# Kernel optimization log

Measured on AMD Instinct MI355X. Metric: run time of the kernel, lower is better.

## Reference

```python
import jax, jax.numpy as jnp
import numpy as np

L, B, T, C, H, V = 6, 8, 1024, 1024, 16, 4096
HS = C // H  # head size = 64


def _ln(x, g, b):
    mu = x.mean(-1, keepdims=True)
    var = ((x - mu) ** 2).mean(-1, keepdims=True)
    return (x - mu) * jax.lax.rsqrt(var + 1e-5) * g + b


def setup_inputs() -> dict:
    key = jax.random.key(0)
    ks = jax.random.split(key, 12)
    s = 0.02
    return {
        "idx": jax.random.randint(ks[0], (B, T), 0, V),
        "tok_emb": jax.random.normal(ks[1], (V, C), jnp.float32) * s,
        "pos_emb": jax.random.normal(ks[2], (T, C), jnp.float32) * s,
        "Wq": jax.random.normal(ks[3], (L, C, C), jnp.float32) * s,
        "Wk": jax.random.normal(ks[4], (L, C, C), jnp.float32) * s,
        "Wv": jax.random.normal(ks[5], (L, C, C), jnp.float32) * s,
        "Wo": jax.random.normal(ks[6], (L, C, C), jnp.float32) * s,
        "bo": jnp.zeros((L, C), jnp.float32),
        "ln1_g": jnp.ones((L, C), jnp.float32),
        "ln1_b": jnp.zeros((L, C), jnp.float32),
        "ln2_g": jnp.ones((L, C), jnp.float32),
        "ln2_b": jnp.zeros((L, C), jnp.float32),
        "W1": jax.random.normal(ks[7], (L, C, 4 * C), jnp.float32) * s,
        "b1": jnp.zeros((L, 4 * C), jnp.float32),
        "W2": jax.random.normal(ks[8], (L, 4 * C, C), jnp.float32) * s,
        "b2": jnp.zeros((L, C), jnp.float32),
        "lnf_g": jnp.ones((C,), jnp.float32),
        "lnf_b": jnp.zeros((C,), jnp.float32),
        "lm_w": jax.random.normal(ks[9], (C, V), jnp.float32) * s,
        "lm_b": jnp.zeros((V,), jnp.float32),
    }


def _gpt(idx, tok_emb, pos_emb, Wq, Wk, Wv, Wo, bo, ln1_g, ln1_b, ln2_g, ln2_b,
         W1, b1, W2, b2, lnf_g, lnf_b, lm_w, lm_b):
    x = tok_emb[idx] + pos_emb[None, :idx.shape[1]]  # (B,T,C)
    mask = jnp.tril(jnp.ones((T, T), bool))
    neg_inf = jnp.float32(-jnp.inf)

    def block(x, p):
        wq, wk, wv, wo, bo_, g1, be1, g2, be2, w1, bb1, w2, bb2 = p
        h = _ln(x, g1, be1)
        # per-head projections (no bias), heads concatenated along feature dim
        q = (h @ wq).reshape(B, T, H, HS)
        k = (h @ wk).reshape(B, T, H, HS)
        v = (h @ wv).reshape(B, T, H, HS)
        # NOTE: faithful to source -- scores are MULTIPLIED by sqrt(head_size)
        att = jnp.einsum('bqhd,bkhd->bhqk', q, k) * (HS ** 0.5)
        att = jnp.where(mask, att, neg_inf)
        p_att = jax.nn.softmax(att, axis=-1)  # dropout is identity at eval
        o = jnp.einsum('bhqk,bkhd->bqhd', p_att, v).reshape(B, T, C)
        x = x + o @ wo + bo_
        h2 = _ln(x, g2, be2)
        x = x + jax.nn.relu(h2 @ w1 + bb1) @ w2 + bb2
        return x, None

    x, _ = jax.lax.scan(
        block, x,
        (Wq, Wk, Wv, Wo, bo, ln1_g, ln1_b, ln2_g, ln2_b, W1, b1, W2, b2))
    x = _ln(x, lnf_g, lnf_b)
    return x @ lm_w + lm_b  # logits (B,T,V)


def reference(idx, tok_emb, pos_emb, Wq, Wk, Wv, Wo, bo, ln1_g, ln1_b, ln2_g,
              ln2_b, W1, b1, W2, b2, lnf_g, lnf_b, lm_w, lm_b):
    return _gpt(idx, tok_emb, pos_emb, Wq, Wk, Wv, Wo, bo, ln1_g, ln1_b,
                ln2_g, ln2_b, W1, b1, W2, b2, lnf_g, lnf_b, lm_w, lm_b)
```

## Files before the change

### kernel.cpp

```cpp
#include <hip/hip_runtime.h>

#define LL 6
#define BB 8
#define TT 1024
#define CC 1024
#define HH 16
#define HS 64
#define VV 4096
#define BT (BB*TT)

typedef __attribute__((ext_vector_type(4))) float f32x4;
typedef __attribute__((ext_vector_type(8))) short bf16x8;

#define RAWBAR() do { \
  asm volatile("s_waitcnt lgkmcnt(0)" ::: "memory"); \
  __builtin_amdgcn_s_barrier(); \
  __builtin_amdgcn_sched_barrier(0); \
} while (0)

__device__ __forceinline__ float bf2f(unsigned short u) {
  union { unsigned int u; float f; } v; v.u = ((unsigned int)u) << 16; return v.f;
}
__device__ __forceinline__ unsigned short rne16(float f) {
  unsigned u = __float_as_uint(f);
  return (unsigned short)((u + 0x7fffu + ((u >> 16) & 1u)) >> 16);
}
__device__ __forceinline__ void gld16(const uint4* g, uint4* l) {
  __builtin_amdgcn_global_load_lds(
      (const __attribute__((address_space(1))) void*)g,
      (__attribute__((address_space(3))) void*)l, 16, 0, 0);
}

__global__ __launch_bounds__(256) void embed_kernel(
    const int* __restrict__ idx, const float* __restrict__ tok,
    const float* __restrict__ pos, float* __restrict__ x) {
  int bt = blockIdx.x;
  int t = bt & (TT - 1);
  int id = idx[bt];
  float4 te = reinterpret_cast<const float4*>(tok)[(size_t)id * (CC/4) + threadIdx.x];
  float4 pe = reinterpret_cast<const float4*>(pos)[(size_t)t * (CC/4) + threadIdx.x];
  float4 r; r.x = te.x+pe.x; r.y = te.y+pe.y; r.z = te.z+pe.z; r.w = te.w+pe.w;
  reinterpret_cast<float4*>(x)[(size_t)bt * (CC/4) + threadIdx.x] = r;
}

struct Oct2 { uint4 p0, p1; };
__device__ __forceinline__ Oct2 split8_rne2(const float* f) {
  unsigned h0[8], h1[8];
  #pragma unroll
  for (int e = 0; e < 8; ++e) {
    h0[e] = rne16(f[e]);
    float r = f[e] - bf2f((unsigned short)h0[e]);
    h1[e] = rne16(r);
  }
  Oct2 o;
  o.p0 = make_uint4(h0[0]|(h0[1]<<16), h0[2]|(h0[3]<<16), h0[4]|(h0[5]<<16), h0[6]|(h0[7]<<16));
  o.p1 = make_uint4(h1[0]|(h1[1]<<16), h1[2]|(h1[3]<<16), h1[4]|(h1[5]<<16), h1[6]|(h1[7]<<16));
  return o;
}
__device__ __forceinline__ uint4 pack8_rne(const float* f) {
  unsigned h[8];
  #pragma unroll
  for (int e = 0; e < 8; ++e) h[e] = rne16(f[e]);
  return make_uint4(h[0]|(h[1]<<16), h[2]|(h[3]<<16), h[4]|(h[5]<<16), h[6]|(h[7]<<16));
}

__global__ __launch_bounds__(256) void lnsplit_kernel(
    const float* __restrict__ x, const float* __restrict__ g,
    const float* __restrict__ b, uint4* __restrict__ outp) {
  __shared__ float red[8];
  __shared__ float rowbuf[1024];
  int row = blockIdx.x, tid = threadIdx.x;
  float4 v = reinterpret_cast<const float4*>(x)[(size_t)row * (CC/4) + tid];
  float s  = v.x+v.y+v.z+v.w;
  float ss = v.x*v.x+v.y*v.y+v.z*v.z+v.w*v.w;
  #pragma unroll
  for (int off = 32; off; off >>= 1) { s += __shfl_xor(s, off); ss += __shfl_xor(ss, off); }
  if ((tid & 63) == 0) { red[tid>>6] = s; red[4+(tid>>6)] = ss; }
  __syncthreads();
  s  = red[0]+red[1]+red[2]+red[3];
  ss = red[4]+red[5]+red[6]+red[7];
  float mu = s * (1.f/CC);
  float rs = rsqrtf(ss*(1.f/CC) - mu*mu + 1e-5f);
  float4 gg = reinterpret_cast<const float4*>(g)[tid];
  float4 bb = reinterpret_cast<const float4*>(b)[tid];
  float4 o;
  o.x = (v.x-mu)*rs*gg.x + bb.x;
  o.y = (v.y-mu)*rs*gg.y + bb.y;
  o.z = (v.z-mu)*rs*gg.z + bb.z;
  o.w = (v.w-mu)*rs*gg.w + bb.w;
  *reinterpret_cast<float4*>(&rowbuf[tid*4]) = o;
  __syncthreads();
  if (tid < 128) {
    const size_t aPS = (size_t)128 * 16 * 512;
    int kt = tid >> 3, sl = tid & 7;
    int r = row & 63, mt = row >> 6;
    float f[8];
    #pragma unroll
    for (int e = 0; e < 8; ++e) f[e] = rowbuf[tid*8 + e];
    size_t di = ((size_t)(mt*16 + kt))*512 + r*8 + (sl ^ (r & 7));
    Oct2 ot = split8_rne2(f);
    outp[di] = ot.p0; outp[aPS+di] = ot.p1;
  }
}

__global__ __launch_bounds__(256) void lnsplit1_kernel(
    const float* __restrict__ x, const float* __restrict__ g,
    const float* __restrict__ b, uint4* __restrict__ outp) {
  __shared__ float red[8];
  __shared__ float rowbuf[1024];
  int row = blockIdx.x, tid = threadIdx.x;
  float4 v = reinterpret_cast<const float4*>(x)[(size_t)row * (CC/4) + tid];
  float s  = v.x+v.y+v.z+v.w;
  float ss = v.x*v.x+v.y*v.y+v.z*v.z+v.w*v.w;
  #pragma unroll
  for (int off = 32; off; off >>= 1) { s += __shfl_xor(s, off); ss += __shfl_xor(ss, off); }
  if ((tid & 63) == 0) { red[tid>>6] = s; red[4+(tid>>6)] = ss; }
  __syncthreads();
  s  = red[0]+red[1]+red[2]+red[3];
  ss = red[4]+red[5]+red[6]+red[7];
  float mu = s * (1.f/CC);
  float rs = rsqrtf(ss*(1.f/CC) - mu*mu + 1e-5f);
  float4 gg = reinterpret_cast<const float4*>(g)[tid];
  float4 bb = reinterpret_cast<const float4*>(b)[tid];
  float4 o;
  o.x = (v.x-mu)*rs*gg.x + bb.x;
  o.y = (v.y-mu)*rs*gg.y + bb.y;
  o.z = (v.z-mu)*rs*gg.z + bb.z;
  o.w = (v.w-mu)*rs*gg.w + bb.w;
  *reinterpret_cast<float4*>(&rowbuf[tid*4]) = o;
  __syncthreads();
  if (tid < 128) {
    int kt = tid >> 3, sl = tid & 7;
    int r = row & 63, mt = row >> 6;
    float f[8];
    #pragma unroll
    for (int e = 0; e < 8; ++e) f[e] = rowbuf[tid*8 + e];
    size_t di = ((size_t)(mt*16 + kt))*512 + r*8 + (sl ^ (r & 7));
    outp[di] = pack8_rne(f);
  }
}

__global__ __launch_bounds__(256) void bsplit4_kernel(
    const float* __restrict__ Wq, const float* __restrict__ Wk,
    const float* __restrict__ Wv, const float* __restrict__ Wo,
    uint4* __restrict__ bsQK, uint4* __restrict__ bsV, uint4* __restrict__ bsO) {
  int z = blockIdx.z;
  const float* Bw = (z == 0) ? Wq : (z == 1) ? Wk : (z == 2) ? Wv : Wo;
  uint4* outp = (z <= 1) ? bsQK : (z == 2) ? bsV : bsO;
  int ntile0 = (z == 1) ? 8 : 0;
  int ntTotal = (z <= 1) ? 16 : 8;
  int ntile = ntile0 + blockIdx.x, kt = blockIdx.y;
  size_t planeStride = (size_t)ntTotal * 16 * 1024;
  int tid = threadIdx.x;
  int bcol = tid & 127, bkcg = tid >> 7;
  #pragma unroll
  for (int g = 0; g < 4; ++g) {
    int kc = bkcg*4 + g;
    float f[8];
    #pragma unroll
    for (int j = 0; j < 8; ++j)
      f[j] = Bw[(size_t)(kt*64 + kc*8 + j) * CC + blockIdx.x*128 + bcol];
    size_t di = (((size_t)ntile * 16 + kt) * 8 + kc) * 128 + bcol;
    Oct2 o = split8_rne2(f);
    outp[di] = o.p0; outp[planeStride+di] = o.p1;
  }
}

template<int NP>
__global__ __launch_bounds__(256) void bsplit_kernel(
    const float* __restrict__ Bw, uint4* __restrict__ outp, int ldb,
    int ntile0, int ntTotal) {
  int ntile = ntile0 + blockIdx.x, kt = blockIdx.y;
  size_t planeStride = (size_t)ntTotal * gridDim.y * 1024;
  int tid = threadIdx.x;
  int bcol = tid & 127, bkcg = tid >> 7;
  #pragma unroll
  for (int g = 0; g < 4; ++g) {
    int kc = bkcg*4 + g;
    float f[8];
    #pragma unroll
    for (int j = 0; j < 8; ++j)
      f[j] = Bw[(size_t)(kt*64 + kc*8 + j) * ldb + blockIdx.x*128 + bcol];
    size_t di = (((size_t)ntile * gridDim.y + kt) * 8 + kc) * 128 + bcol;
    if (NP == 2) {
      Oct2 o = split8_rne2(f);
      outp[di] = o.p0; outp[planeStride+di] = o.p1;
    } else {
      outp[di] = pack8_rne(f);
    }
  }
}

template<int NP, bool ASP, int NM>
__global__ __launch_bounds__(256) void gemm128_kernel(
    const float* __restrict__ A, int lda,
    const uint4* __restrict__ Asp, size_t aPS,
    const uint4* __restrict__ Bs,
    const float* __restrict__ bias, const float* __restrict__ res,
    float* __restrict__ outf, int K, int ldc, int relu,
    int ntile0, int ntTotal, int kt0, int ktTotal, int vtmode,
    uint4* __restrict__ kout) {
  __shared__ uint4 lds_all[NP*2048];
  uint4* lds_a = lds_all;
  uint4* lds_b = lds_all + NP*1024;
  int tid = threadIdx.x;
  int NYd8 = gridDim.y >> 3;
  int li = blockIdx.x + gridDim.x * blockIdx.y;
  int xcd = li & 7, j = li >> 3;
  int by = xcd + 8 * (j % NYd8);
  int bx = j / NYd8;
  int m0 = by * 128;
  int n0 = bx * 128;
  int ntg = ntile0 + bx;
  size_t bPS = (size_t)ntTotal * ktTotal * 1024;
  int lane = tid & 63, w = tid >> 6;
  int wm = w >> 1, wn = w & 1;
  int lr = lane & 15, lk = lane >> 4;
  int nkt = K >> 6;

  f32x4 acc[4][4];
  #pragma unroll
  for (int m = 0; m < 4; ++m)
    #pragma unroll
    for (int n = 0; n < 4; ++n)
      acc[m][n] = (f32x4){0.f, 0.f, 0.f, 0.f};

  for (int kt = 0; kt < nkt; ++kt) {
    if (ASP) {
      #pragma unroll
      for (int p = 0; p < NP; ++p) {
        const uint4* s0 = Asp + p*aPS + ((size_t)(2*by)   * nkt + kt)*512;
        const uint4* s1 = Asp + p*aPS + ((size_t)(2*by+1) * nkt + kt)*512;
        #pragma unroll
        for (int i = 0; i < 2; ++i) {
          int ch = w*2 + i;
          gld16(s0 + ch*64 + lane, &lds_a[p*1024 + ch*64]);
          gld16(s1 + ch*64 + lane, &lds_a[p*1024 + 512 + ch*64]);
        }
      }
    } else {
      #pragma unroll
      for (int i = 0; i < 4; ++i) {
        int c = tid + i * 256;
        int row = c >> 3, sl = c & 7;
        const float4* ap = reinterpret_cast<const float4*>(
            A + (size_t)(m0+row)*lda + kt*64 + sl*8);
        float4 x0 = ap[0], x1 = ap[1];
        float f[8] = {x0.x,x0.y,x0.z,x0.w,x1.x,x1.y,x1.z,x1.w};
        int di = (row>>6)*512 + (row&63)*8 + (sl ^ (row & 7));
        if (NP == 2) {
          Oct2 o = split8_rne2(f);
          lds_a[di] = o.p0; lds_a[1024 + di] = o.p1;
        } else {
          lds_a[di] = pack8_rne(f);
        }
      }
    }
    {
      int ktg = kt0 + kt;
      #pragma unroll
      for (int p = 0; p < NP; ++p) {
        const uint4* sb = Bs + p*bPS + ((size_t)ntg * ktTotal + ktg)*1024;
        #pragma unroll
        for (int i = 0; i < 4; ++i) {
          int ch = w*4 + i;
          gld16(sb + ch*64 + lane, &lds_b[p*1024 + ch*64]);
        }
      }
    }
    __syncthreads();
    #pragma unroll
    for (int ks = 0; ks < 2; ++ks) {
      int kc = ks*4 + lk;
      bf16x8 af[NP][4], bfr[NP][4];
      #pragma unroll
      for (int m = 0; m < 4; ++m) {
        int row = wm*64 + m*16 + lr;
        int si = (row>>6)*512 + (row&63)*8 + (kc ^ (row & 7));
        #pragma unroll
        for (int p = 0; p < NP; ++p)
          af[p][m] = reinterpret_cast<const bf16x8*>(lds_a + p*1024)[si];
      }
      #pragma unroll
      for (int n = 0; n < 4; ++n) {
        int si = kc*128 + wn*64 + n*16 + lr;
        #pragma unroll
        for (int p = 0; p < NP; ++p)
          bfr[p][n] = reinterpret_cast<const bf16x8*>(lds_b + p*1024)[si];
      }
      #pragma unroll
      for (int m = 0; m < 4; ++m)
        #pragma unroll
        for (int n = 0; n < 4; ++n) {
          acc[m][n] = __builtin_amdgcn_mfma_f32_16x16x32_bf16(af[0][m], bfr[0][n], acc[m][n], 0, 0, 0);
          if (NP == 2) {
            acc[m][n] = __builtin_amdgcn_mfma_f32_16x16x32_bf16(af[0][m], bfr[1][n], acc[m][n], 0, 0, 0);
            acc[m][n] = __builtin_amdgcn_mfma_f32_16x16x32_bf16(af[1][m], bfr[0][n], acc[m][n], 0, 0, 0);
            if (NM == 4)
              acc[m][n] = __builtin_amdgcn_mfma_f32_16x16x32_bf16(af[1][m], bfr[1][n], acc[m][n], 0, 0, 0);
          }
        }
    }
    __syncthreads();
  }

  if (vtmode == 1) {
    char* vb = (char*)outf;
    const size_t VPSb = (size_t)2048 * 512 * 16;
    #pragma unroll
    for (int m = 0; m < 4; ++m) {
      int row = m0 + wm*64 + m*16 + lk*4;
      int bq = row >> 10;
      int t  = row & (TT-1);
      int ktile = t >> 6, r = t & 63;
      int kc = r >> 3, toct0 = r & 7;
      #pragma unroll
      for (int n = 0; n < 4; ++n) {
        int col = n0 + wn*64 + n*16 + lr;
        int hh2 = col >> 6, d = col & 63;
        int tile = (bq*HH + hh2)*16 + ktile;
        int vi = kc*64 + ((d ^ (kc<<1)) & 63);
        unsigned p0[4], p1[4];
        #pragma unroll
        for (int j2 = 0; j2 < 4; ++j2) {
          float v = acc[m][n][j2];
          p0[j2] = rne16(v);
          p1[j2] = rne16(v - bf2f((unsigned short)p0[j2]));
        }
        uint2 w0 = make_uint2(p0[0]|(p0[1]<<16), p0[2]|(p0[3]<<16));
        uint2 w1 = make_uint2(p1[0]|(p1[1]<<16), p1[2]|(p1[3]<<16));
        char* base = vb + ((size_t)tile*512 + vi)*16 + toct0*2;
        *reinterpret_cast<uint2*>(base) = w0;
        *reinterpret_cast<uint2*>(base + VPSb) = w1;
      }
    }
  } else if (vtmode == 2) {
    float* bounce = (float*)lds_all;
    #pragma unroll
    for (int m = 0; m < 4; ++m)
      #pragma unroll
      for (int n = 0; n < 4; ++n) {
        int cl = wn*64 + n*16 + lr;
        float bv = bias[n0 + cl];
        #pragma unroll
        for (int j2 = 0; j2 < 4; ++j2) {
          int rl = wm*64 + m*16 + lk*4 + j2;
          bounce[rl*128 + cl] = fmaxf(acc[m][n][j2] + bv, 0.f);
        }
      }
    __syncthreads();
    uint4* a1p = (uint4*)outf;
    const size_t aPSa = (size_t)128 * 32 * 512;
    #pragma unroll
    for (int i = 0; i < 8; ++i) {
      int ot = tid + i*256;
      int r = ot >> 4, o = ot & 15;
      float f[8];
      #pragma unroll
      for (int e = 0; e < 8; ++e) f[e] = bounce[r*128 + o*8 + e];
      Oct2 o2 = split8_rne2(f);
      int mt = 2*by + (r>>6), rs = r & 63;
      int ktg = (n0 >> 6) + (o >> 3), sl = o & 7;
      size_t di = ((size_t)(mt*32 + ktg))*512 + rs*8 + (sl ^ (rs & 7));
      a1p[di] = o2.p0; a1p[aPSa + di] = o2.p1;
    }
  } else if (vtmode == 3 && ntg >= 8) {
    float* bounce = (float*)lds_all;
    #pragma unroll
    for (int m = 0; m < 4; ++m)
      #pragma unroll
      for (int n = 0; n < 4; ++n) {
        int cl = wn*64 + n*16 + lr;
        #pragma unroll
        for (int j2 = 0; j2 < 4; ++j2) {
          int rl = wm*64 + m*16 + lk*4 + j2;
          bounce[rl*128 + cl] = acc[m][n][j2];
        }
      }
    __syncthreads();
    const size_t KPSC = (size_t)2048 * 512;
    int bq = m0 >> 10;
    int kt0tok = (m0 & 1023) >> 6;
    int hh0 = (ntg - 8) * 2;
    #pragma unroll
    for (int i = 0; i < 8; ++i) {
      int u = tid + i*256;
      int r = u >> 4, oct = u & 15;
      int head = oct >> 3, sl = oct & 7;
      float f[8];
      #pragma unroll
      for (int e = 0; e < 8; ++e) f[e] = bounce[r*128 + head*64 + sl*8 + e];
      Oct2 o = split8_rne2(f);
      int rk = r & 63;
      int tile = (bq*HH + hh0 + head)*16 + kt0tok + (r >> 6);
      size_t di = (size_t)tile*512 + rk*8 + (sl ^ (rk & 7));
      kout[di] = o.p0; kout[KPSC + di] = o.p1;
    }
  } else {
    #pragma unroll
    for (int m = 0; m < 4; ++m) {
      #pragma unroll
      for (int n = 0; n < 4; ++n) {
        int col = n0 + wn*64 + n*16 + lr;
        float bv = bias ? bias[col] : 0.f;
        #pragma unroll
        for (int j2 = 0; j2 < 4; ++j2) {
          int row = m0 + wm*64 + m*16 + lk*4 + j2;
          float vv = acc[m][n][j2] + bv;
          if (relu) vv = fmaxf(vv, 0.f);
          size_t off = (size_t)row * ldc + col;
          if (res) vv += res[off];
          outf[off] = vv;
        }
      }
    }
  }
}

__global__ __launch_bounds__(256) void attn_mfma_kernel(
    const float* __restrict__ qf, const uint4* __restrict__ Kp,
    const uint4* __restrict__ Vp, uint4* __restrict__ aout) {
  __shared__ uint4 K_lds[2][512];
  __shared__ uint4 V_lds[2][512];
  __shared__ unsigned P_lds[64*68];
  const size_t KPS = (size_t)2048 * 512;
  const size_t VPS = (size_t)2048 * 512;
  const size_t APS = (size_t)128 * 16 * 512;
  int tid = threadIdx.x, lane = tid & 63, w = tid >> 6;
  int i = blockIdx.x;
  int xcd = i & 7, qm = (i >> 3) & 15, ghi = i >> 7;
  int g = ghi*8 + xcd;
  int b = g >> 4, hh = g & 15, qt = 15 - qm;
  int lr = lane & 15, lk = lane >> 4;
  const size_t tok0 = (size_t)b * TT;
  const int tbase = (b*HH + hh)*16;

  bf16x8 qa[2][2];
  {
    const float* qp = qf + (tok0 + qt*64 + w*16 + lr) * 1024 + hh*HS;
    #pragma unroll
    for (int ks = 0; ks < 2; ++ks) {
      const float4* p4 = reinterpret_cast<const float4*>(qp + ks*32 + lk*8);
      float4 a = p4[0], c = p4[1];
      float f[8] = {a.x,a.y,a.z,a.w,c.x,c.y,c.z,c.w};
      Oct2 ot = split8_rne2(f);
      qa[ks][0] = *reinterpret_cast<bf16x8*>(&ot.p0);
      qa[ks][1] = *reinterpret_cast<bf16x8*>(&ot.p1);
    }
  }

  float mrow[4] = {-3.0e38f,-3.0e38f,-3.0e38f,-3.0e38f};
  float lrow[4] = {0.f,0.f,0.f,0.f};
  f32x4 oac[4];
  #pragma unroll
  for (int n = 0; n < 4; ++n) oac[n] = (f32x4){0.f,0.f,0.f,0.f};

  {
    const uint4* ksrc = Kp + (size_t)tbase*512;
    const uint4* vsrc = Vp + (size_t)tbase*512;
    #pragma unroll
    for (int p = 0; p < 2; ++p)
      #pragma unroll
      for (int i2 = 0; i2 < 2; ++i2) {
        int ch = w*2 + i2;
        gld16(ksrc + p*KPS + ch*64 + lane, &K_lds[p][ch*64]);
        gld16(vsrc + p*VPS + ch*64 + lane, &V_lds[p][ch*64]);
      }
  }

  for (int kt = 0; kt <= qt; ++kt) {
    __syncthreads();

    f32x4 sfr[4];
    #pragma unroll
    for (int nf = 0; nf < 4; ++nf) sfr[nf] = (f32x4){0.f,0.f,0.f,0.f};
    #pragma unroll
    for (int ks = 0; ks < 2; ++ks) {
      int kc = ks*4 + lk;
      #pragma unroll
      for (int nf = 0; nf < 4; ++nf) {
        int row = nf*16 + lr;
        int si = row*8 + (kc ^ (row & 7));
        bf16x8 k0 = *reinterpret_cast<const bf16x8*>(&K_lds[0][si]);
        bf16x8 k1 = *reinterpret_cast<const bf16x8*>(&K_lds[1][si]);
        sfr[nf] = __builtin_amdgcn_mfma_f32_16x16x32_bf16(qa[ks][0], k0, sfr[nf], 0,0,0);
        sfr[nf] = __builtin_amdgcn_mfma_f32_16x16x32_bf16(qa[ks][0], k1, sfr[nf], 0,0,0);
        sfr[nf] = __builtin_amdgcn_mfma_f32_16x16x32_bf16(qa[ks][1], k0, sfr[nf], 0,0,0);
      }
    }
    RAWBAR();

    if (kt < qt) {
      const uint4* ksrc = Kp + (size_t)(tbase + kt + 1)*512;
      #pragma unroll
      for (int p = 0; p < 2; ++p)
        #pragma unroll
        for (int i2 = 0; i2 < 2; ++i2) {
          int ch = w*2 + i2;
          gld16(ksrc + p*KPS + ch*64 + lane, &K_lds[p][ch*64]);
        }
    }

    #pragma unroll
    for (int nf = 0; nf < 4; ++nf)
      #pragma unroll
      for (int j = 0; j < 4; ++j) {
        float s = sfr[nf][j] * 8.0f;
        if (kt == qt && (nf*16 + lr) > (w*16 + lk*4 + j)) s = -3.0e38f;
        sfr[nf][j] = s;
      }
    float alpha[4], tsum[4];
    #pragma unroll
    for (int j = 0; j < 4; ++j) {
      float mx = fmaxf(fmaxf(sfr[0][j], sfr[1][j]), fmaxf(sfr[2][j], sfr[3][j]));
      mx = fmaxf(mx, __shfl_xor(mx, 1));
      mx = fmaxf(mx, __shfl_xor(mx, 2));
      mx = fmaxf(mx, __shfl_xor(mx, 4));
      mx = fmaxf(mx, __shfl_xor(mx, 8));
      float mnew = fmaxf(mrow[j], mx);
      alpha[j] = __expf(mrow[j] - mnew);
      mrow[j] = mnew;
      tsum[j] = 0.f;
    }
    #pragma unroll
    for (int nf = 0; nf < 4; ++nf)
      #pragma unroll
      for (int j = 0; j < 4; ++j) {
        float p = __expf(sfr[nf][j] - mrow[j]);
        tsum[j] += p;
        unsigned u = __float_as_uint(p);
        float r = p - __uint_as_float(u & 0xffff0000u);
        unsigned pw = (u & 0xffff0000u) | (__float_as_uint(r) >> 16);
        int qrow = w*16 + lk*4 + j;
        int kcol = nf*16 + lr;
        P_lds[qrow*68 + (((kcol>>3) ^ (qrow & 7)))*8 + (kcol & 7)] = pw;
      }
    #pragma unroll
    for (int j = 0; j < 4; ++j) {
      float ts = tsum[j];
      ts += __shfl_xor(ts, 1);
      ts += __shfl_xor(ts, 2);
      ts += __shfl_xor(ts, 4);
      ts += __shfl_xor(ts, 8);
      lrow[j] = lrow[j]*alpha[j] + ts;
      oac[0][j] *= alpha[j]; oac[1][j] *= alpha[j];
      oac[2][j] *= alpha[j]; oac[3][j] *= alpha[j];
    }
    RAWBAR();

    #pragma unroll
    for (int ks = 0; ks < 2; ++ks) {
      int kc = ks*4 + lk;
      int prow = w*16 + lr;
      const uint4* pp4 = reinterpret_cast<const uint4*>(
          &P_lds[prow*68 + ((kc ^ (prow & 7)))*8]);
      uint4 pw0 = pp4[0], pw1 = pp4[1];
      uint4 phu, plu;
      phu.x = (pw0.x>>16) | (pw0.y & 0xffff0000u);
      phu.y = (pw0.z>>16) | (pw0.w & 0xffff0000u);
      phu.z = (pw1.x>>16) | (pw1.y & 0xffff0000u);
      phu.w = (pw1.z>>16) | (pw1.w & 0xffff0000u);
      plu.x = (pw0.x & 0xffffu) | (pw0.y << 16);
      plu.y = (pw0.z & 0xffffu) | (pw0.w << 16);
      plu.z = (pw1.x & 0xffffu) | (pw1.y << 16);
      plu.w = (pw1.z & 0xffffu) | (pw1.w << 16);
      bf16x8 ph = *reinterpret_cast<bf16x8*>(&phu);
      bf16x8 pl = *reinterpret_cast<bf16x8*>(&plu);
      #pragma unroll
      for (int nf2 = 0; nf2 < 4; ++nf2) {
        int d = nf2*16 + lr;
        int vi = kc*64 + ((d ^ (kc<<1)) & 63);
        bf16x8 vh = *reinterpret_cast<const bf16x8*>(&V_lds[0][vi]);
        bf16x8 vl = *reinterpret_cast<const bf16x8*>(&V_lds[1][vi]);
        oac[nf2] = __builtin_amdgcn_mfma_f32_16x16x32_bf16(ph, vh, oac[nf2], 0,0,0);
        oac[nf2] = __builtin_amdgcn_mfma_f32_16x16x32_bf16(ph, vl, oac[nf2], 0,0,0);
        oac[nf2] = __builtin_amdgcn_mfma_f32_16x16x32_bf16(pl, vh, oac[nf2], 0,0,0);
      }
    }
    if (kt < qt) {
      RAWBAR();
      const uint4* vsrc = Vp + (size_t)(tbase + kt + 1)*512;
      #pragma unroll
      for (int p = 0; p < 2; ++p)
        #pragma unroll
        for (int i2 = 0; i2 < 2; ++i2) {
          int ch = w*2 + i2;
          gld16(vsrc + p*VPS + ch*64 + lane, &V_lds[p][ch*64]);
        }
    }
  }

  __syncthreads();
  float* Pf = (float*)P_lds;
  #pragma unroll
  for (int j = 0; j < 4; ++j) {
    float inv = 1.0f / lrow[j];
    #pragma unroll
    for (int nf2 = 0; nf2 < 4; ++nf2)
      Pf[(w*16 + lk*4 + j)*68 + nf2*16 + lr] = oac[nf2][j] * inv;
  }
  __syncthreads();
  int mtkt = (b*16 + qt)*16 + hh;
  #pragma unroll
  for (int i2 = 0; i2 < 2; ++i2) {
    int u = tid + i2*256;
    int r = u >> 3, sl = u & 7;
    float f[8];
    #pragma unroll
    for (int e = 0; e < 8; ++e) f[e] = Pf[r*68 + sl*8 + e];
    Oct2 o = split8_rne2(f);
    size_t di = (size_t)mtkt*512 + r*8 + (sl ^ (r & 7));
    aout[di] = o.p0; aout[APS + di] = o.p1;
  }
}

extern "C" void kernel_launch(void* const* d_in, const int* in_sizes, int n_in,
                              void* d_out, int out_size, void* d_ws, size_t ws_size,
                              hipStream_t stream) {
  const int*   idx  = (const int*)d_in[0];
  const float* tok  = (const float*)d_in[1];
  const float* pos  = (const float*)d_in[2];
  const float* Wq   = (const float*)d_in[3];
  const float* Wk   = (const float*)d_in[4];
  const float* Wv   = (const float*)d_in[5];
  const float* Wo   = (const float*)d_in[6];
  const float* bo   = (const float*)d_in[7];
  const float* ln1g = (const float*)d_in[8];
  const float* ln1b = (const float*)d_in[9];
  const float* ln2g = (const float*)d_in[10];
  const float* ln2b = (const float*)d_in[11];
  const float* W1   = (const float*)d_in[12];
  const float* b1   = (const float*)d_in[13];
  const float* W2   = (const float*)d_in[14];
  const float* b2   = (const float*)d_in[15];
  const float* lnfg = (const float*)d_in[16];
  const float* lnfb = (const float*)d_in[17];
  const float* lmw  = (const float*)d_in[18];
  const float* lmb  = (const float*)d_in[19];
  float* out = (float*)d_out;

  char* ob = (char*)d_out;
  float* x  = (float*)ob;
  float* vplanes = (float*)(ob + ((size_t)32<<20));
  float* qf = (float*)(ob + ((size_t)64<<20));
  uint4* Kp = (uint4*)(ob + ((size_t)96<<20));
  float* a1p = (float*)(ob + ((size_t)64<<20));
  char* wsb = (char*)d_ws;
  uint4* aspH  = (uint4*)wsb;
  uint4* bsQK  = (uint4*)(wsb + ((size_t)32<<20));
  uint4* bsV   = (uint4*)(wsb + ((size_t)40<<20));
  uint4* bsO   = (uint4*)(wsb + ((size_t)44<<20));
  uint4* aspH2 = (uint4*)wsb;
  uint4* aspH3 = (uint4*)wsb;
  uint4* bsW1  = (uint4*)(wsb + ((size_t)32<<20));
  uint4* bsW2  = (uint4*)(wsb + ((size_t)48<<20));
  uint4* hfp   = (uint4*)wsb;
  uint4* bsL   = (uint4*)(wsb + ((size_t)32<<20));
  const size_t aPSh = (size_t)128 * 16 * 512;
  const size_t aPSa = (size_t)128 * 32 * 512;

  dim3 blk(256);
  dim3 gQK(16, 64), gV(8, 64), gO(8, 64);
  dim3 gW1(16, 64), gW2(8, 64), gL(32, 64);
  dim3 s4(8, 16, 4), sW1(32, 16), sW2(8, 64), sLM(32, 16);

  embed_kernel<<<BT, blk, 0, stream>>>(idx, tok, pos, x);
  for (int l = 0; l < LL; ++l) {
    const float* Wq_l = Wq + (size_t)l*CC*CC;
    const float* Wk_l = Wk + (size_t)l*CC*CC;
    const float* Wv_l = Wv + (size_t)l*CC*CC;
    const float* Wo_l = Wo + (size_t)l*CC*CC;
    const float* W1_l = W1 + (size_t)l*CC*4*CC;
    const float* W2_l = W2 + (size_t)l*4*CC*CC;
    lnsplit_kernel<<<BT, blk, 0, stream>>>(x, ln1g + (size_t)l*CC, ln1b + (size_t)l*CC, aspH);
    bsplit4_kernel<<<s4, blk, 0, stream>>>(Wq_l, Wk_l, Wv_l, Wo_l, bsQK, bsV, bsO);
    gemm128_kernel<2,true,3><<<gQK, blk, 0, stream>>>(nullptr, 0, aspH, aPSh, bsQK,
        nullptr, nullptr, qf, CC, 1024, 0, 0, 16, 0, 16, 3, Kp);
    gemm128_kernel<2,true,3><<<gV, blk, 0, stream>>>(nullptr, 0, aspH, aPSh, bsV,
        nullptr, nullptr, vplanes, CC, CC, 0, 0, 8, 0, 16, 1, nullptr);
    attn_mfma_kernel<<<BB*HH*16, blk, 0, stream>>>(qf, Kp, (const uint4*)vplanes, aspH2);
    gemm128_kernel<2,true,3><<<gO, blk, 0, stream>>>(nullptr, 0, aspH2, aPSh, bsO,
        bo + (size_t)l*CC, x, x, CC, CC, 0, 0, 8, 0, 16, 0, nullptr);
    lnsplit_kernel<<<BT, blk, 0, stream>>>(x, ln2g + (size_t)l*CC, ln2b + (size_t)l*CC, aspH3);
    bsplit_kernel<2><<<sW1, blk, 0, stream>>>(W1_l, bsW1, 4*CC, 0, 32);
    bsplit_kernel<2><<<sW2, blk, 0, stream>>>(W2_l, bsW2, CC, 0, 8);
    gemm128_kernel<2,true,3><<<gW1, blk, 0, stream>>>(nullptr, 0, aspH3, aPSh, bsW1,
        b1 + (size_t)l*4*CC, nullptr, a1p, CC, 2048, 1, 0, 32, 0, 16, 2, nullptr);
    gemm128_kernel<2,true,3><<<gW2, blk, 0, stream>>>(nullptr, 0, (const uint4*)a1p, aPSa, bsW2,
        b2 + (size_t)l*CC, x, x, 2048, CC, 0, 0, 8, 0, 64, 0, nullptr);
    gemm128_kernel<2,true,3><<<gW1, blk, 0, stream>>>(nullptr, 0, aspH3, aPSh, bsW1,
        b1 + (size_t)l*4*CC + 2048, nullptr, a1p, CC, 2048, 1, 16, 32, 0, 16, 2, nullptr);
    gemm128_kernel<2,true,3><<<gW2, blk, 0, stream>>>(nullptr, 0, (const uint4*)a1p, aPSa, bsW2,
        nullptr, x, x, 2048, CC, 0, 0, 8, 32, 64, 0, nullptr);
  }
  lnsplit1_kernel<<<BT, blk, 0, stream>>>(x, lnfg, lnfb, hfp);
  bsplit_kernel<1><<<sLM, blk, 0, stream>>>(lmw, bsL, VV, 0, 32);
  gemm128_kernel<1,true,1><<<gL, blk, 0, stream>>>(nullptr, 0, hfp, aPSh, bsL,
      lmb, nullptr, out, CC, VV, 0, 0, 32, 0, 16, 0, nullptr);
}
```

Before: 4.271 ms.

## Halve GEMM LDS by reading low-precision planes directly from global memory

```diff
diff --git a/kernel.cpp b/kernel.cpp
--- a/kernel.cpp
+++ b/kernel.cpp
@@ -191,18 +191,17 @@
   }
 }
 
-template<int NP, bool ASP, int NM>
+template<int NP, int NM>
 __global__ __launch_bounds__(256) void gemm128_kernel(
-    const float* __restrict__ A, int lda,
     const uint4* __restrict__ Asp, size_t aPS,
     const uint4* __restrict__ Bs,
     const float* __restrict__ bias, const float* __restrict__ res,
     float* __restrict__ outf, int K, int ldc, int relu,
     int ntile0, int ntTotal, int kt0, int ktTotal, int vtmode,
     uint4* __restrict__ kout) {
-  __shared__ uint4 lds_all[NP*2048];
+  __shared__ uint4 lds_all[2048];
   uint4* lds_a = lds_all;
-  uint4* lds_b = lds_all + NP*1024;
+  uint4* lds_b = lds_all + 1024;
   int tid = threadIdx.x;
   int NYd8 = gridDim.y >> 3;
   int li = blockIdx.x + gridDim.x * blockIdx.y;
@@ -226,78 +225,54 @@
       acc[m][n] = (f32x4){0.f, 0.f, 0.f, 0.f};
 
   for (int kt = 0; kt < nkt; ++kt) {
-    if (ASP) {
-      #pragma unroll
-      for (int p = 0; p < NP; ++p) {
-        const uint4* s0 = Asp + p*aPS + ((size_t)(2*by)   * nkt + kt)*512;
-        const uint4* s1 = Asp + p*aPS + ((size_t)(2*by+1) * nkt + kt)*512;
-        #pragma unroll
-        for (int i = 0; i < 2; ++i) {
-          int ch = w*2 + i;
-          gld16(s0 + ch*64 + lane, &lds_a[p*1024 + ch*64]);
-          gld16(s1 + ch*64 + lane, &lds_a[p*1024 + 512 + ch*64]);
-        }
-      }
-    } else {
+    {
+      const uint4* s0 = Asp + ((size_t)(2*by)   * nkt + kt)*512;
+      const uint4* s1 = Asp + ((size_t)(2*by+1) * nkt + kt)*512;
+      #pragma unroll
+      for (int i = 0; i < 2; ++i) {
+        int ch = w*2 + i;
+        gld16(s0 + ch*64 + lane, &lds_a[ch*64]);
+        gld16(s1 + ch*64 + lane, &lds_a[512 + ch*64]);
+      }
+      const uint4* sb = Bs + ((size_t)ntg * ktTotal + (kt0 + kt))*1024;
       #pragma unroll
       for (int i = 0; i < 4; ++i) {
-        int c = tid + i * 256;
-        int row = c >> 3, sl = c & 7;
-        const float4* ap = reinterpret_cast<const float4*>(
-            A + (size_t)(m0+row)*lda + kt*64 + sl*8);
-        float4 x0 = ap[0], x1 = ap[1];
-        float f[8] = {x0.x,x0.y,x0.z,x0.w,x1.x,x1.y,x1.z,x1.w};
-        int di = (row>>6)*512 + (row&63)*8 + (sl ^ (row & 7));
-        if (NP == 2) {
-          Oct2 o = split8_rne2(f);
-          lds_a[di] = o.p0; lds_a[1024 + di] = o.p1;
-        } else {
-          lds_a[di] = pack8_rne(f);
-        }
-      }
-    }
-    {
-      int ktg = kt0 + kt;
-      #pragma unroll
-      for (int p = 0; p < NP; ++p) {
-        const uint4* sb = Bs + p*bPS + ((size_t)ntg * ktTotal + ktg)*1024;
-        #pragma unroll
-        for (int i = 0; i < 4; ++i) {
-          int ch = w*4 + i;
-          gld16(sb + ch*64 + lane, &lds_b[p*1024 + ch*64]);
-        }
+        int ch = w*4 + i;
+        gld16(sb + ch*64 + lane, &lds_b[ch*64]);
       }
     }
     __syncthreads();
+    const uint4* tA1 = Asp + aPS + ((size_t)(2*by + wm) * nkt + kt)*512;
+    const uint4* tB1 = Bs + bPS + ((size_t)ntg * ktTotal + (kt0 + kt))*1024;
     #pragma unroll
     for (int ks = 0; ks < 2; ++ks) {
       int kc = ks*4 + lk;
-      bf16x8 af[NP][4], bfr[NP][4];
+      bf16x8 af0[4], bf0[4], af1[4], bf1[4];
       #pragma unroll
       for (int m = 0; m < 4; ++m) {
         int row = wm*64 + m*16 + lr;
         int si = (row>>6)*512 + (row&63)*8 + (kc ^ (row & 7));
-        #pragma unroll
-        for (int p = 0; p < NP; ++p)
-          af[p][m] = reinterpret_cast<const bf16x8*>(lds_a + p*1024)[si];
+        af0[m] = reinterpret_cast<const bf16x8*>(lds_a)[si];
+        if (NP == 2)
+          af1[m] = *reinterpret_cast<const bf16x8*>(tA1 + (row&63)*8 + (kc ^ (row & 7)));
       }
       #pragma unroll
       for (int n = 0; n < 4; ++n) {
         int si = kc*128 + wn*64 + n*16 + lr;
-        #pragma unroll
-        for (int p = 0; p < NP; ++p)
-          bfr[p][n] = reinterpret_cast<const bf16x8*>(lds_b + p*1024)[si];
+        bf0[n] = reinterpret_cast<const bf16x8*>(lds_b)[si];
+        if (NP == 2)
+          bf1[n] = *reinterpret_cast<const bf16x8*>(tB1 + si);
       }
       #pragma unroll
       for (int m = 0; m < 4; ++m)
         #pragma unroll
         for (int n = 0; n < 4; ++n) {
-          acc[m][n] = __builtin_amdgcn_mfma_f32_16x16x32_bf16(af[0][m], bfr[0][n], acc[m][n], 0, 0, 0);
+          acc[m][n] = __builtin_amdgcn_mfma_f32_16x16x32_bf16(af0[m], bf0[n], acc[m][n], 0, 0, 0);
           if (NP == 2) {
-            acc[m][n] = __builtin_amdgcn_mfma_f32_16x16x32_bf16(af[0][m], bfr[1][n], acc[m][n], 0, 0, 0);
-            acc[m][n] = __builtin_amdgcn_mfma_f32_16x16x32_bf16(af[1][m], bfr[0][n], acc[m][n], 0, 0, 0);
+            acc[m][n] = __builtin_amdgcn_mfma_f32_16x16x32_bf16(af0[m], bf1[n], acc[m][n], 0, 0, 0);
+            acc[m][n] = __builtin_amdgcn_mfma_f32_16x16x32_bf16(af1[m], bf0[n], acc[m][n], 0, 0, 0);
             if (NM == 4)
-              acc[m][n] = __builtin_amdgcn_mfma_f32_16x16x32_bf16(af[1][m], bfr[1][n], acc[m][n], 0, 0, 0);
+              acc[m][n] = __builtin_amdgcn_mfma_f32_16x16x32_bf16(af1[m], bf1[n], acc[m][n], 0, 0, 0);
           }
         }
     }
@@ -336,65 +311,72 @@
     }
   } else if (vtmode == 2) {
     float* bounce = (float*)lds_all;
-    #pragma unroll
-    for (int m = 0; m < 4; ++m)
-      #pragma unroll
-      for (int n = 0; n < 4; ++n) {
-        int cl = wn*64 + n*16 + lr;
-        float bv = bias[n0 + cl];
-        #pragma unroll
-        for (int j2 = 0; j2 < 4; ++j2) {
-          int rl = wm*64 + m*16 + lk*4 + j2;
-          bounce[rl*128 + cl] = fmaxf(acc[m][n][j2] + bv, 0.f);
-        }
-      }
-    __syncthreads();
     uint4* a1p = (uint4*)outf;
     const size_t aPSa = (size_t)128 * 32 * 512;
     #pragma unroll
-    for (int i = 0; i < 8; ++i) {
-      int ot = tid + i*256;
-      int r = ot >> 4, o = ot & 15;
-      float f[8];
-      #pragma unroll
-      for (int e = 0; e < 8; ++e) f[e] = bounce[r*128 + o*8 + e];
-      Oct2 o2 = split8_rne2(f);
-      int mt = 2*by + (r>>6), rs = r & 63;
-      int ktg = (n0 >> 6) + (o >> 3), sl = o & 7;
-      size_t di = ((size_t)(mt*32 + ktg))*512 + rs*8 + (sl ^ (rs & 7));
-      a1p[di] = o2.p0; a1p[aPSa + di] = o2.p1;
+    for (int pass = 0; pass < 2; ++pass) {
+      __syncthreads();
+      if (wm == pass) {
+        #pragma unroll
+        for (int m = 0; m < 4; ++m)
+          #pragma unroll
+          for (int n = 0; n < 4; ++n) {
+            int cl = wn*64 + n*16 + lr;
+            float bv = bias[n0 + cl];
+            #pragma unroll
+            for (int j2 = 0; j2 < 4; ++j2)
+              bounce[(m*16 + lk*4 + j2)*128 + cl] = fmaxf(acc[m][n][j2] + bv, 0.f);
+          }
+      }
+      __syncthreads();
+      #pragma unroll
+      for (int i = 0; i < 4; ++i) {
+        int ot = tid + i*256;
+        int r = ot >> 4, o = ot & 15;
+        float f[8];
+        #pragma unroll
+        for (int e = 0; e < 8; ++e) f[e] = bounce[r*128 + o*8 + e];
+        Oct2 o2 = split8_rne2(f);
+        int mt = 2*by + pass;
+        int ktg = (n0 >> 6) + (o >> 3), sl = o & 7;
+        size_t di = ((size_t)(mt*32 + ktg))*512 + r*8 + (sl ^ (r & 7));
+        a1p[di] = o2.p0; a1p[aPSa + di] = o2.p1;
+      }
     }
   } else if (vtmode == 3 && ntg >= 8) {
     float* bounce = (float*)lds_all;
-    #pragma unroll
-    for (int m = 0; m < 4; ++m)
-      #pragma unroll
-      for (int n = 0; n < 4; ++n) {
-        int cl = wn*64 + n*16 + lr;
-        #pragma unroll
-        for (int j2 = 0; j2 < 4; ++j2) {
-          int rl = wm*64 + m*16 + lk*4 + j2;
-          bounce[rl*128 + cl] = acc[m][n][j2];
-        }
-      }
-    __syncthreads();
     const size_t KPSC = (size_t)2048 * 512;
     int bq = m0 >> 10;
     int kt0tok = (m0 & 1023) >> 6;
     int hh0 = (ntg - 8) * 2;
     #pragma unroll
-    for (int i = 0; i < 8; ++i) {
-      int u = tid + i*256;
-      int r = u >> 4, oct = u & 15;
-      int head = oct >> 3, sl = oct & 7;
-      float f[8];
-      #pragma unroll
-      for (int e = 0; e < 8; ++e) f[e] = bounce[r*128 + head*64 + sl*8 + e];
-      Oct2 o = split8_rne2(f);
-      int rk = r & 63;
-      int tile = (bq*HH + hh0 + head)*16 + kt0tok + (r >> 6);
-      size_t di = (size_t)tile*512 + rk*8 + (sl ^ (rk & 7));
-      kout[di] = o.p0; kout[KPSC + di] = o.p1;
+    for (int pass = 0; pass < 2; ++pass) {
+      __syncthreads();
+      if (wm == pass) {
+        #pragma unroll
+        for (int m = 0; m < 4; ++m)
+          #pragma unroll
+          for (int n = 0; n < 4; ++n) {
+            int cl = wn*64 + n*16 + lr;
+            #pragma unroll
+            for (int j2 = 0; j2 < 4; ++j2)
+              bounce[(m*16 + lk*4 + j2)*128 + cl] = acc[m][n][j2];
+          }
+      }
+      __syncthreads();
+      #pragma unroll
+      for (int i = 0; i < 4; ++i) {
+        int u = tid + i*256;
+        int r = u >> 4, oct = u & 15;
+        int head = oct >> 3, sl = oct & 7;
+        float f[8];
+        #pragma unroll
+        for (int e = 0; e < 8; ++e) f[e] = bounce[r*128 + head*64 + sl*8 + e];
+        Oct2 o = split8_rne2(f);
+        int tile = (bq*HH + hh0 + head)*16 + kt0tok + pass;
+        size_t di = (size_t)tile*512 + r*8 + (sl ^ (r & 7));
+        kout[di] = o.p0; kout[KPSC + di] = o.p1;
+      }
     }
   } else {
     #pragma unroll
@@ -474,6 +456,7 @@
     f32x4 sfr[4];
     #pragma unroll
     for (int nf = 0; nf < 4; ++nf) sfr[nf] = (f32x4){0.f,0.f,0.f,0.f};
+    __builtin_amdgcn_s_setprio(1);
     #pragma unroll
     for (int ks = 0; ks < 2; ++ks) {
       int kc = ks*4 + lk;
@@ -488,6 +471,7 @@
         sfr[nf] = __builtin_amdgcn_mfma_f32_16x16x32_bf16(qa[ks][1], k0, sfr[nf], 0,0,0);
       }
     }
+    __builtin_amdgcn_s_setprio(0);
     RAWBAR();
 
     if (kt < qt) {
@@ -548,6 +532,7 @@
     }
     RAWBAR();
 
+    __builtin_amdgcn_s_setprio(1);
     #pragma unroll
     for (int ks = 0; ks < 2; ++ks) {
       int kc = ks*4 + lk;
@@ -577,6 +562,7 @@
         oac[nf2] = __builtin_amdgcn_mfma_f32_16x16x32_bf16(pl, vh, oac[nf2], 0,0,0);
       }
     }
+    __builtin_amdgcn_s_setprio(0);
     if (kt < qt) {
       RAWBAR();
       const uint4* vsrc = Vp + (size_t)(tbase + kt + 1)*512;
@@ -674,27 +660,27 @@
     const float* W2_l = W2 + (size_t)l*4*CC*CC;
     lnsplit_kernel<<<BT, blk, 0, stream>>>(x, ln1g + (size_t)l*CC, ln1b + (size_t)l*CC, aspH);
     bsplit4_kernel<<<s4, blk, 0, stream>>>(Wq_l, Wk_l, Wv_l, Wo_l, bsQK, bsV, bsO);
-    gemm128_kernel<2,true,3><<<gQK, blk, 0, stream>>>(nullptr, 0, aspH, aPSh, bsQK,
+    gemm128_kernel<2,3><<<gQK, blk, 0, stream>>>(aspH, aPSh, bsQK,
         nullptr, nullptr, qf, CC, 1024, 0, 0, 16, 0, 16, 3, Kp);
-    gemm128_kernel<2,true,3><<<gV, blk, 0, stream>>>(nullptr, 0, aspH, aPSh, bsV,
+    gemm128_kernel<2,3><<<gV, blk, 0, stream>>>(aspH, aPSh, bsV,
         nullptr, nullptr, vplanes, CC, CC, 0, 0, 8, 0, 16, 1, nullptr);
     attn_mfma_kernel<<<BB*HH*16, blk, 0, stream>>>(qf, Kp, (const uint4*)vplanes, aspH2);
-    gemm128_kernel<2,true,3><<<gO, blk, 0, stream>>>(nullptr, 0, aspH2, aPSh, bsO,
+    gemm128_kernel<2,3><<<gO, blk, 0, stream>>>(aspH2, aPSh, bsO,
         bo + (size_t)l*CC, x, x, CC, CC, 0, 0, 8, 0, 16, 0, nullptr);
     lnsplit_kernel<<<BT, blk, 0, stream>>>(x, ln2g + (size_t)l*CC, ln2b + (size_t)l*CC, aspH3);
     bsplit_kernel<2><<<sW1, blk, 0, stream>>>(W1_l, bsW1, 4*CC, 0, 32);
     bsplit_kernel<2><<<sW2, blk, 0, stream>>>(W2_l, bsW2, CC, 0, 8);
-    gemm128_kernel<2,true,3><<<gW1, blk, 0, stream>>>(nullptr, 0, aspH3, aPSh, bsW1,
+    gemm128_kernel<2,3><<<gW1, blk, 0, stream>>>(aspH3, aPSh, bsW1,
         b1 + (size_t)l*4*CC, nullptr, a1p, CC, 2048, 1, 0, 32, 0, 16, 2, nullptr);
-    gemm128_kernel<2,true,3><<<gW2, blk, 0, stream>>>(nullptr, 0, (const uint4*)a1p, aPSa, bsW2,
+    gemm128_kernel<2,3><<<gW2, blk, 0, stream>>>((const uint4*)a1p, aPSa, bsW2,
         b2 + (size_t)l*CC, x, x, 2048, CC, 0, 0, 8, 0, 64, 0, nullptr);
-    gemm128_kernel<2,true,3><<<gW1, blk, 0, stream>>>(nullptr, 0, aspH3, aPSh, bsW1,
+    gemm128_kernel<2,3><<<gW1, blk, 0, stream>>>(aspH3, aPSh, bsW1,
         b1 + (size_t)l*4*CC + 2048, nullptr, a1p, CC, 2048, 1, 16, 32, 0, 16, 2, nullptr);
-    gemm128_kernel<2,true,3><<<gW2, blk, 0, stream>>>(nullptr, 0, (const uint4*)a1p, aPSa, bsW2,
+    gemm128_kernel<2,3><<<gW2, blk, 0, stream>>>((const uint4*)a1p, aPSa, bsW2,
         nullptr, x, x, 2048, CC, 0, 0, 8, 32, 64, 0, nullptr);
   }
   lnsplit1_kernel<<<BT, blk, 0, stream>>>(x, lnfg, lnfb, hfp);
   bsplit_kernel<1><<<sLM, blk, 0, stream>>>(lmw, bsL, VV, 0, 32);
-  gemm128_kernel<1,true,1><<<gL, blk, 0, stream>>>(nullptr, 0, hfp, aPSh, bsL,
+  gemm128_kernel<1,1><<<gL, blk, 0, stream>>>(hfp, aPSh, bsL,
       lmb, nullptr, out, CC, VV, 0, 0, 32, 0, 16, 0, nullptr);
 }
```

Measured after the change: 4.618 ms. 1.08x slower.
